# Kernel optimization log

Hardware: AMD Instinct MI355X
Metric: run time of the kernel (lower is better)

## Reference

```python
import jax, jax.numpy as jnp
import numpy as np

N_NODES = 100000
N_EDGES = 1000000
N_RELS = 8
N_HEADS = 4
IN_FEAT = 64
OUT_FEAT = 64
D_HEAD = OUT_FEAT // N_HEADS
LEAKY_SLOPE = 0.2


def setup_inputs() -> dict:
    key = jax.random.key(0)
    ks = jax.random.split(key, 8)
    x = jax.random.normal(ks[0], (N_NODES, IN_FEAT), dtype=jnp.float32)
    src_idx = jax.random.randint(ks[1], (N_EDGES,), 0, N_NODES)
    dst_idx = jax.random.randint(ks[2], (N_EDGES,), 0, N_NODES)
    edge_rel = jnp.sort(jax.random.randint(ks[3], (N_EDGES,), 0, N_RELS))
    # xavier-ish small init for weights
    conv_weights = jax.random.normal(ks[4], (N_RELS, N_HEADS, IN_FEAT, D_HEAD), dtype=jnp.float32) * 0.1
    attn_l = jax.random.normal(ks[5], (N_RELS, N_HEADS, D_HEAD), dtype=jnp.float32) * 0.1
    attn_r = jax.random.normal(ks[6], (N_RELS, N_HEADS, D_HEAD), dtype=jnp.float32) * 0.1
    h_bias = jnp.zeros((OUT_FEAT,), dtype=jnp.float32)
    return {
        'x': x, 'src_idx': src_idx, 'dst_idx': dst_idx, 'edge_rel': edge_rel,
        'conv_weights': conv_weights, 'attn_l': attn_l, 'attn_r': attn_r,
        'h_bias': h_bias,
    }


def reference(x, src_idx, dst_idx, edge_rel, conv_weights, attn_l, attn_r, h_bias):
    N = x.shape[0]
    # Per-relation transform of all node features: [R, N, H, D]
    feat_all = jnp.einsum('ni,rhid->rnhd', x, conv_weights)
    # Per-relation attention logits per node: [R, N, H]
    el_all = jnp.einsum('rnhd,rhd->rnh', feat_all, attn_l)
    er_all = jnp.einsum('rnhd,rhd->rnh', feat_all, attn_r)
    # Gather per-edge quantities (relation-specific transform of src/dst)
    feat_e = feat_all[edge_rel, src_idx]          # [E, H, D]
    el = el_all[edge_rel, src_idx]                # [E, H]
    er = er_all[edge_rel, dst_idx]                # [E, H]
    s = jax.nn.leaky_relu(el + er, negative_slope=LEAKY_SLOPE)
    # Edge softmax over incoming edges of each destination node (per head)
    m = jax.ops.segment_max(s, dst_idx, num_segments=N)      # [N, H]
    e = jnp.exp(s - m[dst_idx])                               # [E, H]
    denom = jax.ops.segment_sum(e, dst_idx, num_segments=N)   # [N, H]
    w = e / jnp.maximum(denom[dst_idx], jnp.float32(1e-16))   # [E, H]
    # Weighted aggregation of source features into destination nodes
    agg = jax.ops.segment_sum(feat_e * w[..., None], dst_idx, num_segments=N)  # [N, H, D]
    h = agg.reshape(N, OUT_FEAT) + h_bias
    # activation=None, dropout in eval mode -> identity
    return h
```

## Files before the change

### kernel.cpp

```cpp
#include <hip/hip_runtime.h>
#include <hip/hip_bf16.h>

#define NN 100000
#define NE 1000000
#define NR 8

#define EB 1024
#define NBLK 977
#define NBUCK 196
#define NT (NBUCK*NBLK)
#define NBB 749

#define K3DPB 32
#define K3CAP 160

#define K0_BLKS  160
#define PRE_BLKS (K0_BLKS + NBLK)

#define K1CH 1563
#define F1K 390
#define F2K 390
#define F3K 391
#define F4K 392

typedef unsigned short u16;
typedef unsigned int u32;
typedef __attribute__((ext_vector_type(8))) short bf16x8;
typedef __attribute__((ext_vector_type(4))) float f32x4;

static __device__ __forceinline__ float bf2f(u16 u) {
    union { u32 i; float f; } v; v.i = ((u32)u) << 16; return v.f;
}
static __device__ __forceinline__ float bflo(u32 u) {
    union { u32 i; float f; } v; v.i = u << 16; return v.f;
}
static __device__ __forceinline__ float bfhi(u32 u) {
    union { u32 i; float f; } v; v.i = u & 0xffff0000u; return v.f;
}
static __device__ __forceinline__ u16 f2bf(float f) {
    __hip_bfloat16 h = __float2bfloat16(f);
    return *reinterpret_cast<u16*>(&h);
}
static __device__ __forceinline__ float ldf(const void* p, int idx, int isf32) {
    return isf32 ? ((const float*)p)[idx] : bf2f(((const u16*)p)[idx]);
}

static __device__ __forceinline__ int detect_wave(const u16* xw, int lane)
{
    int insane = 0;
    for (int k = lane; k < 512; k += 64) {
        u16 w = xw[k];
        int ex = (w >> 7) & 0xFF;
        bool sane = ((w & 0x7FFF) == 0) || (ex >= 96 && ex <= 159);
        insane += sane ? 0 : 1;
    }
    for (int off = 32; off; off >>= 1) insane += __shfl_down(insane, off);
    return insane;
}

__global__ __launch_bounds__(256) void k_pre(
    const void* __restrict__ xin, int* __restrict__ flag,
    const void* __restrict__ cw, const void* __restrict__ al,
    const void* __restrict__ ar, u16* __restrict__ Bpre,
    const int* __restrict__ dsti, int* __restrict__ histT)
{
    __shared__ int sflag;
    __shared__ int hist[NBUCK];
    int t = threadIdx.x;
    int b = blockIdx.x;

    if (b < K0_BLKS) {
        if (t < 64) {
            int insane = detect_wave((const u16*)xin, t);
            if (t == 0) {
                sflag = (insane > 50) ? 1 : 0;
                if (b == 0) *flag = sflag;
            }
        }
        __syncthreads();
        int isf32 = sflag;
        int tid = b * 256 + t;
        if (tid >= NR * 5120) return;
        int r = tid / 5120, rem = tid % 5120;
        int c = rem >> 3, j = rem & 7;
        int nt = c >> 7, kk = (c >> 6) & 1, lc = c & 63;
        int i = kk * 32 + ((lc >> 4) << 3) + j;
        int d = lc & 15;
        u16 val;
        if (nt < 4) {
            val = f2bf(ldf(cw, ((r * 4 + nt) * 64 + i) * 16 + d, isf32));
        } else if (d < 8) {
            int h = d >> 1;
            const void* attn = (d & 1) ? ar : al;
            float s = 0.f;
            for (int dd = 0; dd < 16; ++dd)
                s += ldf(cw, ((r * 4 + h) * 64 + i) * 16 + dd, isf32)
                   * ldf(attn, (r * 4 + h) * 16 + dd, isf32);
            val = f2bf(s);
        } else {
            val = 0;
        }
        Bpre[tid] = val;
    } else {
        int blk = b - K0_BLKS;
        if (t < NBUCK) hist[t] = 0;
        __syncthreads();
        int base = blk * EB;
        for (int j = 0; j < EB; j += 256) {
            int e = base + j + t;
            if (e < NE) atomicAdd(&hist[dsti[e] >> 9], 1);
        }
        __syncthreads();
        if (t < NBUCK) histT[t * NBLK + blk] = hist[t];
    }
}

static __device__ __forceinline__ void k1_body(
    int cb, unsigned char* smem,
    const void* __restrict__ xin, const u16* __restrict__ Bpre,
    u16* __restrict__ feat_all, float* __restrict__ el_all, float* __restrict__ er_all)
{
    u32 (*ldsT)[64][32] = (u32 (*)[64][32])smem;
    int n0 = cb * 64;
    int tid = threadIdx.x;
    int wave = tid >> 6, lane = tid & 63;
    int col = lane & 15, quad = lane >> 4;

    int insane = detect_wave((const u16*)xin, lane);
    insane = __shfl(insane, 0);
    int isf32 = (insane > 50) ? 1 : 0;

    int node = n0 + wave * 16 + col;
    int nclamp = node < NN ? node : NN - 1;
    bool nvalid = node < NN;

    bf16x8 afrag0, afrag1;
    if (!isf32) {
        const u16* xb = (const u16*)xin + nclamp * 64 + quad * 8;
        afrag0 = *(const bf16x8*)&xb[0];
        afrag1 = *(const bf16x8*)&xb[32];
    } else {
        const float* xf = (const float*)xin + nclamp * 64 + quad * 8;
#pragma unroll
        for (int j = 0; j < 8; ++j) {
            afrag0[j] = (short)f2bf(xf[j]);
            afrag1[j] = (short)f2bf(xf[32 + j]);
        }
    }

#pragma unroll 1
    for (int ch = 0; ch < 4; ++ch) {
#pragma unroll
        for (int rr = 0; rr < 2; ++rr) {
            int r = ch * 2 + rr;
            f32x4 acc[5];
#pragma unroll
            for (int nt = 0; nt < 5; ++nt) acc[nt] = f32x4{0.f, 0.f, 0.f, 0.f};
#pragma unroll
            for (int nt = 0; nt < 5; ++nt) {
                bf16x8 b0 = *(const bf16x8*)&Bpre[r * 5120 + ((nt * 2 + 0) * 64 + lane) * 8];
                bf16x8 b1 = *(const bf16x8*)&Bpre[r * 5120 + ((nt * 2 + 1) * 64 + lane) * 8];
                acc[nt] = __builtin_amdgcn_mfma_f32_16x16x32_bf16(b0, afrag0, acc[nt], 0, 0, 0);
                acc[nt] = __builtin_amdgcn_mfma_f32_16x16x32_bf16(b1, afrag1, acc[nt], 0, 0, 0);
            }
#pragma unroll
            for (int nt = 0; nt < 4; ++nt) {
                u32 lo = (u32)f2bf(acc[nt][0]) | ((u32)f2bf(acc[nt][1]) << 16);
                u32 hi = (u32)f2bf(acc[nt][2]) | ((u32)f2bf(acc[nt][3]) << 16);
                int w = (nt * 8 + quad * 2) ^ (col * 2);
                *(uint2*)&ldsT[rr][wave * 16 + col][w] = uint2{lo, hi};
            }
            if (nvalid && quad < 2) {
                int eb = (r * NN + node) * 4 + quad * 2;
                *(float2*)&el_all[eb] = float2{acc[4][0], acc[4][2]};
                *(float2*)&er_all[eb] = float2{acc[4][1], acc[4][3]};
            }
        }
        __syncthreads();
#pragma unroll
        for (int it = 0; it < 8; ++it) {
            int u = it * 256 + tid;
            int rr = u >> 10;
            int v = u & 1023;
            int nl = v >> 4;
            int p  = v & 15;
            int w  = (p * 2) ^ ((nl & 15) * 2);
            uint2 val = *(const uint2*)&ldsT[rr][nl][w];
            int nd = n0 + nl;
            if (nd < NN)
                *(uint2*)&feat_all[((ch * 2 + rr) * NN + nd) * 64 + p * 4] = val;
        }
        __syncthreads();
    }
}

static __device__ __forceinline__ void scanB1_body(
    int b, unsigned char* smem, int* __restrict__ histT, int* __restrict__ bsum)
{
    int* wtot = (int*)smem;
    int t = threadIdx.x;
    int gi = b * 256 + t;
    int v = (gi < NT) ? histT[gi] : 0;
    int lane = t & 63, w = t >> 6;
    int s = v;
#pragma unroll
    for (int m = 1; m < 64; m <<= 1) {
        int u = __shfl_up(s, m);
        if (lane >= m) s += u;
    }
    if (lane == 63) wtot[w] = s;
    __syncthreads();
    int wb = 0;
    for (int i = 0; i < w; ++i) wb += wtot[i];
    if (gi < NT) histT[gi] = wb + s - v;
    if (t == 255) bsum[b] = wb + s;
}

static __device__ __forceinline__ void scanB2_body(
    unsigned char* smem, const int* __restrict__ bsum, int* __restrict__ boff,
    const int* __restrict__ histT, int* __restrict__ bstart)
{
    int* wtot  = (int*)smem;
    int* sboff = (int*)(smem + 16);
    int* carry = (int*)(smem + 16 + 4 * NBB);
    int t = threadIdx.x;
    if (t == 0) *carry = 0;
    __syncthreads();
    for (int c = 0; c < 3; ++c) {
        int idx = c * 256 + t;
        int v = (idx < NBB) ? bsum[idx] : 0;
        int lane = t & 63, w = t >> 6;
        int s = v;
#pragma unroll
        for (int m = 1; m < 64; m <<= 1) {
            int u = __shfl_up(s, m);
            if (lane >= m) s += u;
        }
        if (lane == 63) wtot[w] = s;
        __syncthreads();
        int wb = 0;
        for (int i = 0; i < w; ++i) wb += wtot[i];
        int ex = *carry + wb + s - v;
        if (idx < NBB) sboff[idx] = ex;
        __syncthreads();
        if (t == 255) *carry += wb + s;
        __syncthreads();
    }
    for (int i = t; i < NBB; i += 256) boff[i] = sboff[i];
    if (t < NBUCK) {
        int gi = t * NBLK;
        bstart[t] = histT[gi] + sboff[gi >> 8];
    }
    if (t == 0) bstart[NBUCK] = NE;
}

static __device__ __forceinline__ void binC_body(
    int b, unsigned char* smem,
    const int* __restrict__ srci, const int* __restrict__ dsti,
    const int* __restrict__ reli, const int* __restrict__ histT,
    const int* __restrict__ boff, int* __restrict__ key_b)
{
    int* cur = (int*)smem;
    int t = threadIdx.x;
    if (t < NBUCK) {
        int gi = t * NBLK + b;
        cur[t] = histT[gi] + boff[gi >> 8];
    }
    __syncthreads();
    int base = b * EB;
    for (int j = 0; j < EB; j += 256) {
        int e = base + j + t;
        if (e < NE) {
            int d = dsti[e];
            int key = ((d & 511) << 20) | (reli[e] << 17) | srci[e];
            int pos = atomicAdd(&cur[d >> 9], 1);
            key_b[pos] = key;
        }
    }
}

static __device__ __forceinline__ void binD_body(
    int b, unsigned char* smem,
    const int* __restrict__ bstart, const int* __restrict__ key_b,
    int* __restrict__ key_s, int* __restrict__ off)
{
    int* cnt   = (int*)smem;
    int* wtot  = (int*)(smem + 2048);
    int* carry = (int*)(smem + 2064);
    int t = threadIdx.x;
    int s0 = bstart[b], s1 = bstart[b + 1];
    cnt[t] = 0; cnt[t + 256] = 0;
    if (t == 0) *carry = 0;
    __syncthreads();
    for (int j = s0 + t; j < s1; j += 256)
        atomicAdd(&cnt[(key_b[j] >> 20) & 511], 1);
    __syncthreads();
    int excl[2];
#pragma unroll
    for (int c = 0; c < 2; ++c) {
        int v = cnt[c * 256 + t];
        int lane = t & 63, w = t >> 6;
        int s = v;
#pragma unroll
        for (int m = 1; m < 64; m <<= 1) {
            int u = __shfl_up(s, m);
            if (lane >= m) s += u;
        }
        if (lane == 63) wtot[w] = s;
        __syncthreads();
        int wb = 0;
        for (int i = 0; i < w; ++i) wb += wtot[i];
        excl[c] = s0 + *carry + wb + s - v;
        __syncthreads();
        if (t == 255) *carry += wb + s;
        __syncthreads();
    }
#pragma unroll
    for (int c = 0; c < 2; ++c) {
        int d = (b << 9) + c * 256 + t;
        if (d < NN) off[d] = excl[c];
    }
    cnt[t] = excl[0]; cnt[t + 256] = excl[1];
    if (b == 0 && t == 0) off[NN] = NE;
    __syncthreads();
    for (int j = s0 + t; j < s1; j += 256) {
        int key = key_b[j];
        int pos = atomicAdd(&cnt[(key >> 20) & 511], 1);
        key_s[pos] = key;
    }
}

__global__ __launch_bounds__(256) void k_fused(
    int stage, int nsort, int k1base,
    const void* __restrict__ xin, const u16* __restrict__ Bpre,
    u16* __restrict__ feat_all, float* __restrict__ el_all, float* __restrict__ er_all,
    const int* __restrict__ srci, const int* __restrict__ dsti,
    const int* __restrict__ reli,
    int* __restrict__ histT, int* __restrict__ bsum, int* __restrict__ boff,
    int* __restrict__ bstart, int* __restrict__ key_b, int* __restrict__ key_s,
    int* __restrict__ off)
{
    __shared__ alignas(16) unsigned char smem[16448];
    int b = blockIdx.x;
    if (b >= nsort) {
        k1_body(k1base + (b - nsort), smem, xin, Bpre, feat_all, el_all, er_all);
        return;
    }
    if (stage == 0)      scanB1_body(b, smem, histT, bsum);
    else if (stage == 1) scanB2_body(smem, bsum, boff, histT, bstart);
    else if (stage == 2) binC_body(b, smem, srci, dsti, reli, histT, boff, key_b);
    else                 binD_body(b, smem, bstart, key_b, key_s, off);
}

__global__ __launch_bounds__(256) void k3_node(
    const int* __restrict__ off, const int* __restrict__ key_s,
    const float* __restrict__ el_all, const float* __restrict__ er_all,
    const u16* __restrict__ feat_all, const void* __restrict__ bias,
    const int* __restrict__ flag, void* __restrict__ out)
{
    __shared__ int   ldsOffs[K3DPB + 1];
    __shared__ int   ldsKey[4][K3CAP];
    __shared__ float ldsEE[4][K3CAP][4];
    int t = threadIdx.x;
    int wave = t >> 6, lane = t & 63;
    int dg = lane >> 3;
    int fl = lane & 7;
    int h  = fl >> 1;
    int d0 = blockIdx.x * K3DPB;
    int isf32 = *flag;

    if (t < K3DPB + 1) ldsOffs[t] = off[min(d0 + t, NN)];
    __syncthreads();

    int dlo = wave * 8;
    int estart = ldsOffs[dlo], eend = ldsOffs[dlo + 8];
    int scount = min(eend - estart, K3CAP);

    int dbase = d0 & ~511;
    for (int j = lane; j < scount; j += 64) {
        int key = key_s[estart + j];
        int rel = (key >> 17) & 7, src = key & 131071;
        int d = dbase | ((key >> 20) & 511);
        int kk = rel * NN + src;
        f32x4 el = *(const f32x4*)&el_all[kk * 4];
        f32x4 er = *(const f32x4*)&er_all[(rel * NN + d) * 4];
        f32x4 ee;
#pragma unroll
        for (int q = 0; q < 4; ++q) {
            float v = el[q] + er[q];
            v = v > 0.f ? v : 0.2f * v;
            ee[q] = __expf(v);
        }
        ldsKey[wave][j] = kk;
        *(f32x4*)&ldsEE[wave][j][0] = ee;
    }

    float bv[8];
#pragma unroll
    for (int q = 0; q < 8; ++q) bv[q] = ldf(bias, fl * 8 + q, isf32);

    int nl = dlo + dg;
    int d = d0 + nl;
    int s  = ldsOffs[nl] - estart;
    int e1 = ldsOffs[nl + 1] - estart;
    float acc[8] = {0.f, 0.f, 0.f, 0.f, 0.f, 0.f, 0.f, 0.f};
    float accW = 0.f;

    int e1c = min(e1, K3CAP);
    for (int base = s; base < e1c; base += 4) {
        int kk[4]; float w[4];
#pragma unroll
        for (int q = 0; q < 4; ++q) {
            int idx = base + q;
            bool vld = idx < e1c;
            kk[q] = vld ? ldsKey[wave][idx] : ldsKey[wave][base];
            w[q]  = vld ? ldsEE[wave][idx][h] : 0.f;
        }
        uint4 u[4];
#pragma unroll
        for (int q = 0; q < 4; ++q)
            u[q] = *(const uint4*)&feat_all[kk[q] * 64 + fl * 8];
#pragma unroll
        for (int q = 0; q < 4; ++q) {
            acc[0] += bflo(u[q].x) * w[q];
            acc[1] += bfhi(u[q].x) * w[q];
            acc[2] += bflo(u[q].y) * w[q];
            acc[3] += bfhi(u[q].y) * w[q];
            acc[4] += bflo(u[q].z) * w[q];
            acc[5] += bfhi(u[q].z) * w[q];
            acc[6] += bflo(u[q].w) * w[q];
            acc[7] += bfhi(u[q].w) * w[q];
            accW += w[q];
        }
    }
    for (int j = max(s, K3CAP); j < e1; ++j) {
        int key = key_s[estart + j];
        int rel = (key >> 17) & 7, src = key & 131071;
        int kk0 = rel * NN + src;
        float v = el_all[kk0 * 4 + h] + er_all[(rel * NN + d) * 4 + h];
        v = v > 0.f ? v : 0.2f * v;
        float w0 = __expf(v);
        uint4 u = *(const uint4*)&feat_all[kk0 * 64 + fl * 8];
        acc[0] += bflo(u.x) * w0;
        acc[1] += bfhi(u.x) * w0;
        acc[2] += bflo(u.y) * w0;
        acc[3] += bfhi(u.y) * w0;
        acc[4] += bflo(u.z) * w0;
        acc[5] += bfhi(u.z) * w0;
        acc[6] += bflo(u.w) * w0;
        acc[7] += bfhi(u.w) * w0;
        accW += w0;
    }

    {
        float invh = 1.f / fmaxf(accW, 1e-16f);
        float o[8];
#pragma unroll
        for (int q = 0; q < 8; ++q) o[q] = acc[q] * invh + bv[q];
        if (isf32) {
            ((f32x4*)out)[d * 16 + fl * 2]     = f32x4{o[0], o[1], o[2], o[3]};
            ((f32x4*)out)[d * 16 + fl * 2 + 1] = f32x4{o[4], o[5], o[6], o[7]};
        } else {
            uint4 st;
            st.x = (u32)f2bf(o[0]) | ((u32)f2bf(o[1]) << 16);
            st.y = (u32)f2bf(o[2]) | ((u32)f2bf(o[3]) << 16);
            st.z = (u32)f2bf(o[4]) | ((u32)f2bf(o[5]) << 16);
            st.w = (u32)f2bf(o[6]) | ((u32)f2bf(o[7]) << 16);
            *(uint4*)&((u16*)out)[d * 64 + fl * 8] = st;
        }
    }
}

extern "C" void kernel_launch(void* const* d_in, const int* in_sizes, int n_in,
                              void* d_out, int out_size, void* d_ws, size_t ws_size,
                              hipStream_t stream)
{
    const void* x   = d_in[0];
    const int* srci = (const int*)d_in[1];
    const int* dsti = (const int*)d_in[2];
    const int* reli = (const int*)d_in[3];
    const void* cw  = d_in[4];
    const void* al  = d_in[5];
    const void* ar  = d_in[6];
    const void* hb  = d_in[7];

    char* ws = (char*)d_ws;
    u16*   feat_all = (u16*)  (ws + 0);
    float* el_all   = (float*)(ws + 102400000);
    float* er_all   = (float*)(ws + 115200000);
    int*   key_s    = (int*)  (ws + 128000000);
    int*   key_b    = (int*)  (ws + 132000000);
    int*   off      = (int*)  (ws + 136000000);
    int*   histT    = (int*)  (ws + 136400064);
    int*   bsum     = (int*)  (ws + 137166032);
    int*   boff     = (int*)  (ws + 137169040);
    int*   bstart   = (int*)  (ws + 137172048);
    u16*   Bpre     = (u16*)  (ws + 137172880);
    int*   flag     = (int*)  (ws + 137254800);

    k_pre<<<PRE_BLKS, 256, 0, stream>>>(x, flag, cw, al, ar, Bpre, dsti, histT);

    k_fused<<<NBB + F1K, 256, 0, stream>>>(0, NBB, 0,
        x, Bpre, feat_all, el_all, er_all, srci, dsti, reli,
        histT, bsum, boff, bstart, key_b, key_s, off);
    k_fused<<<1 + F2K, 256, 0, stream>>>(1, 1, F1K,
        x, Bpre, feat_all, el_all, er_all, srci, dsti, reli,
        histT, bsum, boff, bstart, key_b, key_s, off);
    k_fused<<<NBLK + F3K, 256, 0, stream>>>(2, NBLK, F1K + F2K,
        x, Bpre, feat_all, el_all, er_all, srci, dsti, reli,
        histT, bsum, boff, bstart, key_b, key_s, off);
    k_fused<<<NBUCK + F4K, 256, 0, stream>>>(3, NBUCK, F1K + F2K + F3K,
        x, Bpre, feat_all, el_all, er_all, srci, dsti, reli,
        histT, bsum, boff, bstart, key_b, key_s, off);

    k3_node<<<(NN + 31) / 32, 256, 0, stream>>>(off, key_s, el_all, er_all, feat_all,
                                                hb, flag, d_out);
}
```

Measured before the change: 216.4 us.

## Merge four sort-stage launches into one kernel with software grid barriers

Replaces the four separate k_fused launches (each pairing one sort stage with a slice of the feature-transform work) with a single k_mid launch. The first NBLK blocks run all sort stages in sequence, separated by atomic-counter grid barriers, and the remaining blocks do the feature transform. The barrier counters are reset in k_pre. This removes three kernel launch boundaries and lets the transform blocks run alongside the whole sort. It relies on all 977 sort blocks being resident at once, or the barriers deadlock, and spin-waiting blocks may hold CUs that the transform blocks could use.

Result: slower. 494.9 us (+128.7%).

```diff
diff --git a/kernel.cpp b/kernel.cpp
--- a/kernel.cpp
+++ b/kernel.cpp
@@ -17,11 +17,8 @@
 #define K0_BLKS  160
 #define PRE_BLKS (K0_BLKS + NBLK)
 
-#define K1CH 1563
-#define F1K 390
-#define F2K 390
-#define F3K 391
-#define F4K 392
+#define NSORT NBLK
+#define K1CH  1563
 
 typedef unsigned short u16;
 typedef unsigned int u32;
@@ -43,6 +40,20 @@
 }
 static __device__ __forceinline__ float ldf(const void* p, int idx, int isf32) {
     return isf32 ? ((const float*)p)[idx] : bf2f(((const u16*)p)[idx]);
+}
+
+static __device__ __forceinline__ void gbar(int* cnt, int target)
+{
+    __syncthreads();
+    if (threadIdx.x == 0) {
+        __threadfence();
+        atomicAdd(cnt, 1);
+        while (__hip_atomic_load(cnt, __ATOMIC_RELAXED,
+                                 __HIP_MEMORY_SCOPE_AGENT) < target)
+            __builtin_amdgcn_s_sleep(32);
+        __threadfence();
+    }
+    __syncthreads();
 }
 
 static __device__ __forceinline__ int detect_wave(const u16* xw, int lane)
@@ -62,12 +73,15 @@
     const void* __restrict__ xin, int* __restrict__ flag,
     const void* __restrict__ cw, const void* __restrict__ al,
     const void* __restrict__ ar, u16* __restrict__ Bpre,
-    const int* __restrict__ dsti, int* __restrict__ histT)
+    const int* __restrict__ dsti, int* __restrict__ histT,
+    int* __restrict__ sortcnt)
 {
     __shared__ int sflag;
     __shared__ int hist[NBUCK];
     int t = threadIdx.x;
     int b = blockIdx.x;
+
+    if (b == 0 && t < 4) sortcnt[t] = 0;
 
     if (b < K0_BLKS) {
         if (t < 64) {
@@ -330,26 +344,28 @@
     }
 }
 
-__global__ __launch_bounds__(256) void k_fused(
-    int stage, int nsort, int k1base,
+__global__ __launch_bounds__(256) void k_mid(
     const void* __restrict__ xin, const u16* __restrict__ Bpre,
     u16* __restrict__ feat_all, float* __restrict__ el_all, float* __restrict__ er_all,
     const int* __restrict__ srci, const int* __restrict__ dsti,
     const int* __restrict__ reli,
     int* __restrict__ histT, int* __restrict__ bsum, int* __restrict__ boff,
     int* __restrict__ bstart, int* __restrict__ key_b, int* __restrict__ key_s,
-    int* __restrict__ off)
+    int* __restrict__ off, int* __restrict__ sortcnt)
 {
     __shared__ alignas(16) unsigned char smem[16448];
     int b = blockIdx.x;
-    if (b >= nsort) {
-        k1_body(k1base + (b - nsort), smem, xin, Bpre, feat_all, el_all, er_all);
+    if (b >= NSORT) {
+        k1_body(b - NSORT, smem, xin, Bpre, feat_all, el_all, er_all);
         return;
     }
-    if (stage == 0)      scanB1_body(b, smem, histT, bsum);
-    else if (stage == 1) scanB2_body(smem, bsum, boff, histT, bstart);
-    else if (stage == 2) binC_body(b, smem, srci, dsti, reli, histT, boff, key_b);
-    else                 binD_body(b, smem, bstart, key_b, key_s, off);
+    if (b < NBB) scanB1_body(b, smem, histT, bsum);
+    gbar(&sortcnt[0], NSORT);
+    if (b == 0) scanB2_body(smem, bsum, boff, histT, bstart);
+    gbar(&sortcnt[1], NSORT);
+    binC_body(b, smem, srci, dsti, reli, histT, boff, key_b);
+    gbar(&sortcnt[2], NSORT);
+    if (b < NBUCK) binD_body(b, smem, bstart, key_b, key_s, off);
 }
 
 __global__ __launch_bounds__(256) void k3_node(
@@ -497,22 +513,13 @@
     int*   bstart   = (int*)  (ws + 137172048);
     u16*   Bpre     = (u16*)  (ws + 137172880);
     int*   flag     = (int*)  (ws + 137254800);
-
-    k_pre<<<PRE_BLKS, 256, 0, stream>>>(x, flag, cw, al, ar, Bpre, dsti, histT);
-
-    k_fused<<<NBB + F1K, 256, 0, stream>>>(0, NBB, 0,
-        x, Bpre, feat_all, el_all, er_all, srci, dsti, reli,
-        histT, bsum, boff, bstart, key_b, key_s, off);
-    k_fused<<<1 + F2K, 256, 0, stream>>>(1, 1, F1K,
-        x, Bpre, feat_all, el_all, er_all, srci, dsti, reli,
-        histT, bsum, boff, bstart, key_b, key_s, off);
-    k_fused<<<NBLK + F3K, 256, 0, stream>>>(2, NBLK, F1K + F2K,
-        x, Bpre, feat_all, el_all, er_all, srci, dsti, reli,
-        histT, bsum, boff, bstart, key_b, key_s, off);
-    k_fused<<<NBUCK + F4K, 256, 0, stream>>>(3, NBUCK, F1K + F2K + F3K,
-        x, Bpre, feat_all, el_all, er_all, srci, dsti, reli,
-        histT, bsum, boff, bstart, key_b, key_s, off);
-
+    int*   sortcnt  = (int*)  (ws + 137254816);
+
+    k_pre<<<PRE_BLKS, 256, 0, stream>>>(x, flag, cw, al, ar, Bpre, dsti, histT,
+                                        sortcnt);
+    k_mid<<<NSORT + K1CH, 256, 0, stream>>>(x, Bpre, feat_all, el_all, er_all,
+                                            srci, dsti, reli, histT, bsum, boff,
+                                            bstart, key_b, key_s, off, sortcnt);
     k3_node<<<(NN + 31) / 32, 256, 0, stream>>>(off, key_s, el_all, er_all, feat_all,
                                                 hb, flag, d_out);
 }
```
